# Optimization experiments

Measured on AMD Instinct MI355X. Metric: run time of the kernel, lower is better.

The kernel has to match this reference:

```python
import jax, jax.numpy as jnp
import numpy as np

TOP_K = 400
IGNORE = 255


def setup_inputs() -> dict:
    key = jax.random.key(0)
    k = jax.random.split(key, 6)
    B, C, H, W = 16, 3, 768, 768
    D, He, We = 64, 192, 192
    return {
        "outputs": jax.random.normal(k[0], (B, C, H, W), jnp.float32),
        "embeddings": jax.random.normal(k[1], (B, D, He, We), jnp.float32),
        "class_labels": jax.random.randint(k[2], (B, H, W), 0, 3, jnp.int32),
        "outputs_aug": jax.random.normal(k[3], (B, C, H, W), jnp.float32),
        "embeddings_aug": jax.random.normal(k[4], (B, D, He, We), jnp.float32),
        "class_labels_aug": jax.random.randint(k[5], (B, H, W), 0, 3, jnp.int32),
    }


def _nearest_down(x, He, We):
    # torch F.interpolate(mode='nearest') with integer downscale factor == strided slice
    sH = x.shape[-2] // He
    sW = x.shape[-1] // We
    return x[..., ::sH, ::sW]


def _forward(outputs, embeddings, outputs_aug, embeddings_aug, class_labels):
    B, C, H, W = outputs.shape
    D, He, We = embeddings.shape[1], embeddings.shape[2], embeddings.shape[3]

    # --- CrossEntropy(ignore_index=255), per-sample mean, averaged over batch ---
    logp = jax.nn.log_softmax(outputs, axis=1)                      # [B,C,H,W]
    valid = class_labels != IGNORE                                   # [B,H,W]
    lbl = jnp.where(valid, class_labels, 0).astype(jnp.int32)
    nll = -jnp.take_along_axis(logp, lbl[:, None], axis=1)[:, 0]     # [B,H,W]
    loss_ce = ((nll * valid).sum((1, 2)) / jnp.maximum(valid.sum((1, 2)), 1)).mean()

    # --- confidence / prediction maps, downsampled to embedding resolution ---
    def conf_seg(o):
        p = jax.nn.softmax(o, axis=1)
        return p.max(axis=1), p.argmax(axis=1)

    conf, seg = conf_seg(outputs)
    conf_a, seg_a = conf_seg(outputs_aug)
    segd = _nearest_down(seg, He, We)
    confd = _nearest_down(conf, He, We)
    segd_a = _nearest_down(seg_a, He, We)
    confd_a = _nearest_down(conf_a, He, We)

    def per_sample(emb, emb_a, sg, cf, sg_a, cf_a):
        ef = emb.reshape(D, -1)                                      # [D,P]
        efa = emb_a.reshape(D, -1)
        n = ef / jnp.linalg.norm(ef, axis=0, keepdims=True)          # unit columns
        na = efa / jnp.linalg.norm(efa, axis=0, keepdims=True)
        sgf, cff = sg.ravel(), cf.ravel()
        sgfa, cffa = sg_a.ravel(), cf_a.ravel()

        # ---- class 1 (ths=0.8): sort masked pixels by channel-mean, take top_k ----
        m1 = (sgf == 1) & (cff > 0.8)
        m1a = (sgfa == 1) & (cffa > 0.8)

        def topk_sel(nrm, ef_, m):
            keyv = jnp.where(m, ef_.mean(0), jnp.inf)  # unmasked -> +inf, sorted last
            idx = jnp.argsort(keyv)[:TOP_K]
            return nrm[:, idx]                         # [D,TOP_K], already unit-norm

        s1 = topk_sel(n, ef, m1)
        s1a = topk_sel(na, efa, m1a)
        d1 = 1.0 - (s1.T @ s1a).mean()                 # mean pairwise cosine distance
        v1 = (m1.sum() > TOP_K) & (m1a.sum() > TOP_K)

        # ---- class 2 (ths=0.6): all masked pixels; mean over pairs of cos-sim
        # equals dot of masked means of unit vectors (exact identity) ----
        m2 = (sgf == 2) & (cff > 0.6)
        m2a = (sgfa == 2) & (cffa > 0.6)
        mu = (n * m2).sum(1) / jnp.maximum(m2.sum(), 1)
        mua = (na * m2a).sum(1) / jnp.maximum(m2a.sum(), 1)
        d2 = 1.0 - mu @ mua
        v2 = (m2.sum() > 0) & (m2a.sum() > 0)
        return d1, v1, d2, v2

    d1, v1, d2, v2 = jax.vmap(per_sample)(embeddings, embeddings_aug, segd, confd, segd_a, confd_a)
    cnt = v1.sum() + v2.sum()
    loss_matching = (jnp.where(v1, d1, 0.0).sum() + jnp.where(v2, d2, 0.0).sum()) / jnp.maximum(cnt, 1)
    loss = loss_ce + 2.0 * loss_matching
    return loss, loss_ce, loss_matching


def reference(outputs, embeddings, class_labels, outputs_aug, embeddings_aug, class_labels_aug):
    # class_labels_aug does not enter the loss in the original code (aug CE is built but never added)
    return _forward(outputs, embeddings, outputs_aug, embeddings_aug, class_labels)
```

## Files before the change

### kernel.cpp

```cpp
#include <hip/hip_runtime.h>
#include <cstdint>
#include <cstddef>

#define Bn 16
#define Cn 3
#define Hn 768
#define Wn 768
#define Dn 64
#define HEn 192
#define WEn 192
#define Pn (HEn * WEn)
#define HWn (Hn * Wn)
#define TOPK 400
#define SENTK 0xFFFFFFFFu
#define PAD 16
#define PXB 128

struct Ws {
  float ce_sum[Bn][PAD];
  int   ce_cnt[Bn][PAD];
  int   cnt1[2][Bn][PAD];
  int   cnt2[2][Bn][PAD];
  float mu2[2][Bn][Dn][PAD];
  float mu1[2][Bn][Dn][PAD];
  int   nsel[2][Bn];
  int   idxl[2][Bn][TOPK];
  unsigned keys[2][Bn][Pn];
};
#define INIT_WORDS (256 + 256 + 512 + 512 + 32768 + 32768)
static_assert(offsetof(Ws, nsel) == (size_t)INIT_WORDS * 4, "ws layout");
static_assert(sizeof(Ws) < (size_t)6 * 1024 * 1024, "ws small");

__global__ void init_kernel(Ws* ws) {
  unsigned* w = (unsigned*)ws;
  int t = blockIdx.x * blockDim.x + threadIdx.x;
  for (int i = t; i < INIT_WORDS; i += gridDim.x * blockDim.x) w[i] = 0u;
}

__device__ __forceinline__ float wave_sum_f(float s) {
#pragma unroll
  for (int off = 32; off; off >>= 1) s += __shfl_down(s, off);
  return s;
}
__device__ __forceinline__ int wave_sum_i(int s) {
#pragma unroll
  for (int off = 32; off; off >>= 1) s += __shfl_down(s, off);
  return s;
}

__global__ void ce_kernel(const float* __restrict__ out, const int* __restrict__ lab,
                          Ws* __restrict__ ws) {
  int b = blockIdx.y;
  const int NT = 144 * 256;
  int t = blockIdx.x * 256 + threadIdx.x;
  const float* base = out + (size_t)b * Cn * HWn;
  const int* lb_base = lab + (size_t)b * HWn;
  float s = 0.f; int c = 0;
#pragma unroll
  for (int it = 0; it < 4; it++) {
    int p4 = (t + it * NT) * 4;
    float4 a0 = *(const float4*)(base + p4);
    float4 a1 = *(const float4*)(base + HWn + p4);
    float4 a2 = *(const float4*)(base + 2 * HWn + p4);
    int4 lb = *(const int4*)(lb_base + p4);
    float x0s[4] = {a0.x, a0.y, a0.z, a0.w};
    float x1s[4] = {a1.x, a1.y, a1.z, a1.w};
    float x2s[4] = {a2.x, a2.y, a2.z, a2.w};
    int ls[4] = {lb.x, lb.y, lb.z, lb.w};
#pragma unroll
    for (int k = 0; k < 4; k++) {
      int l = ls[k];
      if (l != 255) {
        float x0 = x0s[k], x1 = x1s[k], x2 = x2s[k];
        float m = fmaxf(x0, fmaxf(x1, x2));
        float lse = m + __logf(__expf(x0 - m) + __expf(x1 - m) + __expf(x2 - m));
        float xl = (l == 0) ? x0 : ((l == 1) ? x1 : x2);
        s += lse - xl;
        c += 1;
      }
    }
  }
  s = wave_sum_f(s);
  c = wave_sum_i(c);
  __shared__ float ss[4];
  __shared__ int sc[4];
  int wid = threadIdx.x >> 6;
  if ((threadIdx.x & 63) == 0) { ss[wid] = s; sc[wid] = c; }
  __syncthreads();
  if (threadIdx.x == 0) {
    atomicAdd(&ws->ce_sum[b][0], ss[0] + ss[1] + ss[2] + ss[3]);
    atomicAdd(&ws->ce_cnt[b][0], sc[0] + sc[1] + sc[2] + sc[3]);
  }
}

__global__ void main_kernel(const float* __restrict__ o0, const float* __restrict__ o1,
                            const float* __restrict__ e0, const float* __restrict__ e1,
                            Ws* __restrict__ ws) {
  int arr = blockIdx.z;
  int b = blockIdx.y;
  int lane = threadIdx.x & 63, wv = threadIdx.x >> 6;
  int p0 = blockIdx.x * PXB;
  int pa = p0 + 2 * lane;

  const float* e = (arr ? e1 : e0) + ((size_t)b * Dn + wv * 16) * Pn;
  float va[16], vb[16];
  float sum0 = 0.f, sum1 = 0.f, sq0 = 0.f, sq1 = 0.f;
#pragma unroll
  for (int k = 0; k < 16; k++) {
    float2 x = *(const float2*)(e + (size_t)k * Pn + pa);
    va[k] = x.x; vb[k] = x.y;
    sum0 += x.x; sq0 += x.x * x.x;
    sum1 += x.y; sq1 += x.y * x.y;
  }

  __shared__ float psum[4][PXB], psq[4][PXB];
  __shared__ float sscale[PXB];
  *(float2*)&psum[wv][2 * lane] = make_float2(sum0, sum1);
  *(float2*)&psq[wv][2 * lane] = make_float2(sq0, sq1);
  __syncthreads();

  if (wv == 0) {
    const float* o = (arr ? o1 : o0) + (size_t)b * Cn * HWn;
    unsigned kb[2]; float sc[2]; bool m1f[2], m2f[2];
#pragma unroll
    for (int h = 0; h < 2; h++) {
      int px = 2 * lane + h;
      int p = p0 + px;
      float ts = psum[0][px] + psum[1][px] + psum[2][px] + psum[3][px];
      float tq = psq[0][px] + psq[1][px] + psq[2][px] + psq[3][px];
      int i = p / WEn, j = p - i * WEn;
      int q = (4 * i) * Wn + 4 * j;
      float x0 = o[q], x1 = o[q + HWn], x2 = o[q + 2 * HWn];
      int sgc = 0; float m = x0;
      if (x1 > m) { m = x1; sgc = 1; }
      if (x2 > m) { m = x2; sgc = 2; }
      float conf = 1.0f / (__expf(x0 - m) + __expf(x1 - m) + __expf(x2 - m));
      bool m1 = (sgc == 1) && (conf > 0.8f);
      bool m2 = (sgc == 2) && (conf > 0.6f);
      unsigned kbv = SENTK;
      if (m1) {
        unsigned u = __float_as_uint(ts);
        kbv = (u & 0x80000000u) ? ~u : (u | 0x80000000u);
        if (kbv == SENTK) kbv--;
      }
      kb[h] = kbv;
      sc[h] = m2 ? rsqrtf(tq) : 0.f;
      m1f[h] = m1; m2f[h] = m2;
    }
    *(uint2*)&ws->keys[arr][b][pa] = make_uint2(kb[0], kb[1]);
    *(float2*)&sscale[2 * lane] = make_float2(sc[0], sc[1]);
    unsigned long long b10 = __ballot(m1f[0]), b11 = __ballot(m1f[1]);
    unsigned long long b20 = __ballot(m2f[0]), b21 = __ballot(m2f[1]);
    if (lane == 0) {
      int c1 = (int)__popcll(b10) + (int)__popcll(b11);
      int c2 = (int)__popcll(b20) + (int)__popcll(b21);
      if (c1) atomicAdd(&ws->cnt1[arr][b][0], c1);
      if (c2) atomicAdd(&ws->cnt2[arr][b][0], c2);
    }
  }
  __syncthreads();

  float2 s2 = *(const float2*)&sscale[2 * lane];
  float rv = 0.f;
#pragma unroll
  for (int k = 0; k < 16; k++) {
    float x = va[k] * s2.x + vb[k] * s2.y;
#pragma unroll
    for (int off = 1; off < 64; off <<= 1) x += __shfl_xor(x, off);
    if (lane == k) rv = x;
  }
  if (lane < 16 && rv != 0.f)
    atomicAdd(&ws->mu2[arr][b][wv * 16 + lane][0], rv);
}

__global__ void __launch_bounds__(1024) select_kernel(Ws* __restrict__ ws) {
  int arr = blockIdx.x >> 4;
  int b = blockIdx.x & 15;
  int tid = threadIdx.x;
  const uint4* __restrict__ keys4 = (const uint4*)ws->keys[arr][b];
  int c1 = ws->cnt1[arr][b][0];
  if (c1 <= TOPK) {
    if (tid == 0) ws->nsel[arr][b] = 0;
    return;
  }
  __shared__ int hist[2048];
  __shared__ int super[128];
  __shared__ int tieBuf[256];
  __shared__ unsigned sPrefix;
  __shared__ int sKRem, nBelow, nTie;
  if (tid == 0) { sPrefix = 0u; sKRem = TOPK; }

  const int shifts[3] = {21, 10, 0};
  const unsigned bmask[3] = {2047u, 2047u, 1023u};
  const int nbins[3] = {2048, 2048, 1024};

  for (int lvl = 0; lvl < 3; lvl++) {
    hist[tid] = 0;
    hist[tid + 1024] = 0;
    __syncthreads();
    unsigned pref = sPrefix;
    int shift = shifts[lvl];
    unsigned bm = bmask[lvl];
#pragma unroll
    for (int it = 0; it < 9; it++) {
      uint4 u4 = keys4[it * 1024 + tid];
      unsigned us[4] = {u4.x, u4.y, u4.z, u4.w};
#pragma unroll
      for (int k = 0; k < 4; k++) {
        unsigned u = us[k];
        if (u == SENTK) continue;
        if (lvl == 1 && (u >> 21) != (pref >> 21)) continue;
        if (lvl == 2 && (u >> 10) != (pref >> 10)) continue;
        atomicAdd(&hist[(u >> shift) & bm], 1);
      }
    }
    __syncthreads();
    int SB = nbins[lvl] >> 7;
    if (tid < 128) {
      int s = 0;
      for (int k = 0; k < SB; k++) s += hist[tid * SB + k];
      super[tid] = s;
    }
    __syncthreads();
    if (tid == 0) {
      int k = sKRem, cum = 0, sb = 127;
      for (int t = 0; t < 128; t++) {
        if (cum + super[t] >= k) { sb = t; break; }
        cum += super[t];
      }
      int j = sb * SB + SB - 1;
      for (int t = sb * SB; t < sb * SB + SB; t++) {
        if (cum + hist[t] >= k) { j = t; k -= cum; break; }
        cum += hist[t];
      }
      sKRem = k;
      sPrefix = pref | ((unsigned)j << shift);
    }
    __syncthreads();
  }
  unsigned T = sPrefix;
  int kRem = sKRem;
  if (tid == 0) { nBelow = 0; nTie = 0; }
  __syncthreads();
  int* idxl = ws->idxl[arr][b];
#pragma unroll
  for (int it = 0; it < 9; it++) {
    uint4 u4 = keys4[it * 1024 + tid];
    unsigned us[4] = {u4.x, u4.y, u4.z, u4.w};
#pragma unroll
    for (int k = 0; k < 4; k++) {
      unsigned u = us[k];
      int p = (it * 1024 + tid) * 4 + k;
      if (u < T) {
        int pos = atomicAdd(&nBelow, 1);
        if (pos < TOPK) idxl[pos] = p;
      } else if (u == T) {
        int tp = atomicAdd(&nTie, 1);
        if (tp < 256) tieBuf[tp] = p;
      }
    }
  }
  __syncthreads();
  if (tid == 0) {
    int nb = nBelow;
    int tn = nTie < 256 ? nTie : 256;
    int take = kRem < tn ? kRem : tn;
    for (int r = 0; r < take; r++) {
      int mi = r;
      for (int t = r + 1; t < tn; t++)
        if (tieBuf[t] < tieBuf[mi]) mi = t;
      int tmp = tieBuf[r]; tieBuf[r] = tieBuf[mi]; tieBuf[mi] = tmp;
      if (nb + r < TOPK) idxl[nb + r] = tieBuf[r];
    }
    int ns = nb + take;
    ws->nsel[arr][b] = ns > TOPK ? TOPK : ns;
  }
}

__global__ void accum1_kernel(const float* __restrict__ e0, const float* __restrict__ e1,
                              Ws* __restrict__ ws) {
  int arr = blockIdx.y >> 4;
  int b = blockIdx.y & 15;
  int chunk = blockIdx.x;
  int ns = ws->nsel[arr][b];
  if (chunk * 64 >= ns) return;
  int lane = threadIdx.x & 63, wv = threadIdx.x >> 6;
  int t = chunk * 64 + lane;
  bool valid = t < ns;
  int p = valid ? ws->idxl[arr][b][t] : 0;
  const float* e = (arr ? e1 : e0) + ((size_t)b * Dn + wv * 16) * Pn;
  float v[16]; float sq = 0.f;
#pragma unroll
  for (int k = 0; k < 16; k++) {
    float x = e[(size_t)k * Pn + p];
    v[k] = x; sq += x * x;
  }
  __shared__ float psq[4][64];
  psq[wv][lane] = sq;
  __syncthreads();
  float tq = psq[0][lane] + psq[1][lane] + psq[2][lane] + psq[3][lane];
  float s = valid ? rsqrtf(tq) : 0.f;
  float rv = 0.f;
#pragma unroll
  for (int k = 0; k < 16; k++) {
    float x = v[k] * s;
#pragma unroll
    for (int off = 1; off < 64; off <<= 1) x += __shfl_xor(x, off);
    if (lane == k) rv = x;
  }
  if (lane < 16 && rv != 0.f)
    atomicAdd(&ws->mu1[arr][b][wv * 16 + lane][0], rv);
}

__global__ void final_kernel(Ws* __restrict__ ws, float* __restrict__ out) {
  int t = threadIdx.x;
  float ce = 0.f, num = 0.f;
  int cnt = 0;
  if (t < Bn) {
    int cc = ws->ce_cnt[t][0];
    ce = ws->ce_sum[t][0] / (float)(cc > 1 ? cc : 1);
    int c1o = ws->cnt1[0][t][0], c1a = ws->cnt1[1][t][0];
    if (c1o > TOPK && c1a > TOPK) {
      float dot = 0.f;
      for (int d = 0; d < Dn; d++) dot += ws->mu1[0][t][d][0] * ws->mu1[1][t][d][0];
      num += 1.f - dot / ((float)TOPK * (float)TOPK);
      cnt += 1;
    }
    int c2o = ws->cnt2[0][t][0], c2a = ws->cnt2[1][t][0];
    if (c2o > 0 && c2a > 0) {
      float dot = 0.f;
      for (int d = 0; d < Dn; d++) dot += ws->mu2[0][t][d][0] * ws->mu2[1][t][d][0];
      float den = (float)(c2o > 1 ? c2o : 1) * (float)(c2a > 1 ? c2a : 1);
      num += 1.f - dot / den;
      cnt += 1;
    }
  }
#pragma unroll
  for (int off = 32; off; off >>= 1) {
    ce += __shfl_down(ce, off);
    num += __shfl_down(num, off);
    cnt += __shfl_down(cnt, off);
  }
  if (t == 0) {
    float loss_ce = ce / (float)Bn;
    float lm = num / (float)(cnt > 1 ? cnt : 1);
    out[0] = loss_ce + 2.f * lm;
    out[1] = loss_ce;
    out[2] = lm;
  }
}

extern "C" void kernel_launch(void* const* d_in, const int* in_sizes, int n_in,
                              void* d_out, int out_size, void* d_ws, size_t ws_size,
                              hipStream_t stream) {
  const float* outputs      = (const float*)d_in[0];
  const float* embeddings   = (const float*)d_in[1];
  const int*   class_labels = (const int*)d_in[2];
  const float* outputs_aug  = (const float*)d_in[3];
  const float* emb_aug      = (const float*)d_in[4];
  Ws* ws = (Ws*)d_ws;
  float* out = (float*)d_out;

  init_kernel<<<32, 256, 0, stream>>>(ws);
  ce_kernel<<<dim3(144, Bn), 256, 0, stream>>>(outputs, class_labels, ws);
  main_kernel<<<dim3(Pn / PXB, Bn, 2), 256, 0, stream>>>(outputs, outputs_aug,
                                                         embeddings, emb_aug, ws);
  select_kernel<<<32, 1024, 0, stream>>>(ws);
  accum1_kernel<<<dim3(7, 32), 256, 0, stream>>>(embeddings, emb_aug, ws);
  final_kernel<<<1, 64, 0, stream>>>(ws, out);
}
```

Baseline: 532.4 us.

## Restructure main kernel into per-wave pixel loop with register accumulation of class-2 means

The main kernel now has each wave handle 256 pixels over 8 iterations, with each half-wave reading 32 embedding channels per pixel. Channel sums and squared norms are combined with a single cross-half shuffle, which replaces the shared-memory reduction and both block-wide barriers. Class-2 contributions are accumulated in registers across iterations and reduced once per wave, cutting the per-block shuffle reductions and atomics on mu2. The cost is higher register pressure from 64 live floats per thread, a far smaller grid (36x16x2 blocks), and only 32-pixel-wide coalesced loads per row.

Result: no change. 540.4 us (+1.5%).

```diff
diff --git a/kernel.cpp b/kernel.cpp
--- a/kernel.cpp
+++ b/kernel.cpp
@@ -14,7 +14,6 @@
 #define TOPK 400
 #define SENTK 0xFFFFFFFFu
 #define PAD 16
-#define PXB 128
 
 struct Ws {
   float ce_sum[Bn][PAD];
@@ -93,41 +92,31 @@
   }
 }
 
-__global__ void main_kernel(const float* __restrict__ o0, const float* __restrict__ o1,
-                            const float* __restrict__ e0, const float* __restrict__ e1,
-                            Ws* __restrict__ ws) {
-  int arr = blockIdx.z;
-  int b = blockIdx.y;
-  int lane = threadIdx.x & 63, wv = threadIdx.x >> 6;
-  int p0 = blockIdx.x * PXB;
-  int pa = p0 + 2 * lane;
-
-  const float* e = (arr ? e1 : e0) + ((size_t)b * Dn + wv * 16) * Pn;
-  float va[16], vb[16];
-  float sum0 = 0.f, sum1 = 0.f, sq0 = 0.f, sq1 = 0.f;
-#pragma unroll
-  for (int k = 0; k < 16; k++) {
-    float2 x = *(const float2*)(e + (size_t)k * Pn + pa);
-    va[k] = x.x; vb[k] = x.y;
-    sum0 += x.x; sq0 += x.x * x.x;
-    sum1 += x.y; sq1 += x.y * x.y;
-  }
-
-  __shared__ float psum[4][PXB], psq[4][PXB];
-  __shared__ float sscale[PXB];
-  *(float2*)&psum[wv][2 * lane] = make_float2(sum0, sum1);
-  *(float2*)&psq[wv][2 * lane] = make_float2(sq0, sq1);
-  __syncthreads();
-
-  if (wv == 0) {
-    const float* o = (arr ? o1 : o0) + (size_t)b * Cn * HWn;
-    unsigned kb[2]; float sc[2]; bool m1f[2], m2f[2];
-#pragma unroll
-    for (int h = 0; h < 2; h++) {
-      int px = 2 * lane + h;
-      int p = p0 + px;
-      float ts = psum[0][px] + psum[1][px] + psum[2][px] + psum[3][px];
-      float tq = psq[0][px] + psq[1][px] + psq[2][px] + psq[3][px];
+__global__ void __launch_bounds__(256, 4)
+main_kernel(const float* __restrict__ o0, const float* __restrict__ o1,
+            const float* __restrict__ e0, const float* __restrict__ e1,
+            Ws* __restrict__ ws) {
+  const int arr = blockIdx.z;
+  const int b = blockIdx.y;
+  const int lane = threadIdx.x & 63, wv = threadIdx.x >> 6;
+  const int wave_id = blockIdx.x * 4 + wv;
+  const int l31 = lane & 31;
+  const int half = lane >> 5;
+  const float* e = (arr ? e1 : e0) + (size_t)(b * Dn + half * 32) * (size_t)Pn;
+  const float* o = (arr ? o1 : o0) + (size_t)b * Cn * HWn;
+  unsigned* __restrict__ keys = ws->keys[arr][b];
+
+  float acc[32];
+#pragma unroll
+  for (int k = 0; k < 32; k++) acc[k] = 0.f;
+  int c1a = 0, c2a = 0;
+
+#pragma unroll 1
+  for (int g = 0; g < 8; g++) {
+    const int p = wave_id * 256 + g * 32 + l31;
+
+    bool m1 = false, m2 = false;
+    if (half == 0) {
       int i = p / WEn, j = p - i * WEn;
       int q = (4 * i) * Wn + 4 * j;
       float x0 = o[q], x1 = o[q + HWn], x2 = o[q + 2 * HWn];
@@ -135,42 +124,55 @@
       if (x1 > m) { m = x1; sgc = 1; }
       if (x2 > m) { m = x2; sgc = 2; }
       float conf = 1.0f / (__expf(x0 - m) + __expf(x1 - m) + __expf(x2 - m));
-      bool m1 = (sgc == 1) && (conf > 0.8f);
-      bool m2 = (sgc == 2) && (conf > 0.6f);
+      m1 = (sgc == 1) && (conf > 0.8f);
+      m2 = (sgc == 2) && (conf > 0.6f);
+    }
+
+    const float* ep = e + p;
+    float v[32];
+    float s = 0.f, sq = 0.f;
+#pragma unroll
+    for (int k = 0; k < 32; k++) {
+      float x = ep[(size_t)k * Pn];
+      v[k] = x; s += x; sq += x * x;
+    }
+    s += __shfl_xor(s, 32);
+    sq += __shfl_xor(sq, 32);
+
+    float sc = 0.f;
+    if (half == 0) {
       unsigned kbv = SENTK;
       if (m1) {
-        unsigned u = __float_as_uint(ts);
+        unsigned u = __float_as_uint(s);
         kbv = (u & 0x80000000u) ? ~u : (u | 0x80000000u);
         if (kbv == SENTK) kbv--;
       }
-      kb[h] = kbv;
-      sc[h] = m2 ? rsqrtf(tq) : 0.f;
-      m1f[h] = m1; m2f[h] = m2;
-    }
-    *(uint2*)&ws->keys[arr][b][pa] = make_uint2(kb[0], kb[1]);
-    *(float2*)&sscale[2 * lane] = make_float2(sc[0], sc[1]);
-    unsigned long long b10 = __ballot(m1f[0]), b11 = __ballot(m1f[1]);
-    unsigned long long b20 = __ballot(m2f[0]), b21 = __ballot(m2f[1]);
-    if (lane == 0) {
-      int c1 = (int)__popcll(b10) + (int)__popcll(b11);
-      int c2 = (int)__popcll(b20) + (int)__popcll(b21);
-      if (c1) atomicAdd(&ws->cnt1[arr][b][0], c1);
-      if (c2) atomicAdd(&ws->cnt2[arr][b][0], c2);
-    }
-  }
-  __syncthreads();
-
-  float2 s2 = *(const float2*)&sscale[2 * lane];
-  float rv = 0.f;
-#pragma unroll
-  for (int k = 0; k < 16; k++) {
-    float x = va[k] * s2.x + vb[k] * s2.y;
-#pragma unroll
-    for (int off = 1; off < 64; off <<= 1) x += __shfl_xor(x, off);
-    if (lane == k) rv = x;
-  }
-  if (lane < 16 && rv != 0.f)
-    atomicAdd(&ws->mu2[arr][b][wv * 16 + lane][0], rv);
+      keys[p] = kbv;
+      if (m2) sc = rsqrtf(sq);
+    }
+    float scu = __shfl_xor(sc, 32);
+    if (half) sc = scu;
+
+#pragma unroll
+    for (int k = 0; k < 32; k++) acc[k] = fmaf(v[k], sc, acc[k]);
+
+    unsigned long long b1 = __ballot(m1), b2 = __ballot(m2);
+    c1a += (int)__popcll(b1);
+    c2a += (int)__popcll(b2);
+  }
+
+#pragma unroll
+  for (int k = 0; k < 32; k++) {
+    float x = acc[k];
+#pragma unroll
+    for (int off = 1; off < 32; off <<= 1) x += __shfl_xor(x, off);
+    if (l31 == k && x != 0.f)
+      atomicAdd(&ws->mu2[arr][b][half * 32 + k][0], x);
+  }
+  if (lane == 0) {
+    if (c1a) atomicAdd(&ws->cnt1[arr][b][0], c1a);
+    if (c2a) atomicAdd(&ws->cnt2[arr][b][0], c2a);
+  }
 }
 
 __global__ void __launch_bounds__(1024) select_kernel(Ws* __restrict__ ws) {
@@ -363,8 +365,8 @@
 
   init_kernel<<<32, 256, 0, stream>>>(ws);
   ce_kernel<<<dim3(144, Bn), 256, 0, stream>>>(outputs, class_labels, ws);
-  main_kernel<<<dim3(Pn / PXB, Bn, 2), 256, 0, stream>>>(outputs, outputs_aug,
-                                                         embeddings, emb_aug, ws);
+  main_kernel<<<dim3(36, Bn, 2), 256, 0, stream>>>(outputs, outputs_aug,
+                                                   embeddings, emb_aug, ws);
   select_kernel<<<32, 1024, 0, stream>>>(ws);
   accum1_kernel<<<dim3(7, 32), 256, 0, stream>>>(embeddings, emb_aug, ws);
   final_kernel<<<1, 64, 0, stream>>>(ws, out);
```

## Process four pixel chunks per block in main_kernel with register accumulation

Applied to the files above, without the earlier changes.

Each main_kernel block now loops over four 128-pixel chunks and accumulates the class-2 masked embedding sums in registers. The 16 shuffle reductions and the mu2 and count atomics are therefore issued once per block instead of once per chunk. The next chunk's logits are prefetched while the current chunk is processed, and launch bounds are set to 256 threads with 6 blocks per unit. The grid becomes four times smaller, which lowers parallelism and adds a serial loop with extra barriers per block.

Result: no change. 526.0 us (-1.2%).

```diff
diff --git a/kernel.cpp b/kernel.cpp
--- a/kernel.cpp
+++ b/kernel.cpp
@@ -15,6 +15,7 @@
 #define SENTK 0xFFFFFFFFu
 #define PAD 16
 #define PXB 128
+#define CHUNKS 4
 
 struct Ws {
   float ce_sum[Bn][PAD];
@@ -93,84 +94,117 @@
   }
 }
 
-__global__ void main_kernel(const float* __restrict__ o0, const float* __restrict__ o1,
-                            const float* __restrict__ e0, const float* __restrict__ e1,
-                            Ws* __restrict__ ws) {
+__global__ void __launch_bounds__(256, 6)
+main_kernel(const float* __restrict__ o0, const float* __restrict__ o1,
+            const float* __restrict__ e0, const float* __restrict__ e1,
+            Ws* __restrict__ ws) {
   int arr = blockIdx.z;
   int b = blockIdx.y;
   int lane = threadIdx.x & 63, wv = threadIdx.x >> 6;
-  int p0 = blockIdx.x * PXB;
-  int pa = p0 + 2 * lane;
-
+  int base_p = blockIdx.x * (PXB * CHUNKS);
+
+  const float* o = (arr ? o1 : o0) + (size_t)b * Cn * HWn;
   const float* e = (arr ? e1 : e0) + ((size_t)b * Dn + wv * 16) * Pn;
-  float va[16], vb[16];
-  float sum0 = 0.f, sum1 = 0.f, sq0 = 0.f, sq1 = 0.f;
-#pragma unroll
-  for (int k = 0; k < 16; k++) {
-    float2 x = *(const float2*)(e + (size_t)k * Pn + pa);
-    va[k] = x.x; vb[k] = x.y;
-    sum0 += x.x; sq0 += x.x * x.x;
-    sum1 += x.y; sq1 += x.y * x.y;
-  }
 
   __shared__ float psum[4][PXB], psq[4][PXB];
   __shared__ float sscale[PXB];
-  *(float2*)&psum[wv][2 * lane] = make_float2(sum0, sum1);
-  *(float2*)&psq[wv][2 * lane] = make_float2(sq0, sq1);
-  __syncthreads();
-
+
+  float acc[16];
+#pragma unroll
+  for (int k = 0; k < 16; k++) acc[k] = 0.f;
+  int c1a = 0, c2a = 0;
+
+  float px0[2], px1[2], px2[2];
   if (wv == 0) {
-    const float* o = (arr ? o1 : o0) + (size_t)b * Cn * HWn;
-    unsigned kb[2]; float sc[2]; bool m1f[2], m2f[2];
 #pragma unroll
     for (int h = 0; h < 2; h++) {
-      int px = 2 * lane + h;
-      int p = p0 + px;
-      float ts = psum[0][px] + psum[1][px] + psum[2][px] + psum[3][px];
-      float tq = psq[0][px] + psq[1][px] + psq[2][px] + psq[3][px];
+      int p = base_p + 2 * lane + h;
       int i = p / WEn, j = p - i * WEn;
       int q = (4 * i) * Wn + 4 * j;
-      float x0 = o[q], x1 = o[q + HWn], x2 = o[q + 2 * HWn];
-      int sgc = 0; float m = x0;
-      if (x1 > m) { m = x1; sgc = 1; }
-      if (x2 > m) { m = x2; sgc = 2; }
-      float conf = 1.0f / (__expf(x0 - m) + __expf(x1 - m) + __expf(x2 - m));
-      bool m1 = (sgc == 1) && (conf > 0.8f);
-      bool m2 = (sgc == 2) && (conf > 0.6f);
-      unsigned kbv = SENTK;
-      if (m1) {
-        unsigned u = __float_as_uint(ts);
-        kbv = (u & 0x80000000u) ? ~u : (u | 0x80000000u);
-        if (kbv == SENTK) kbv--;
-      }
-      kb[h] = kbv;
-      sc[h] = m2 ? rsqrtf(tq) : 0.f;
-      m1f[h] = m1; m2f[h] = m2;
-    }
-    *(uint2*)&ws->keys[arr][b][pa] = make_uint2(kb[0], kb[1]);
-    *(float2*)&sscale[2 * lane] = make_float2(sc[0], sc[1]);
-    unsigned long long b10 = __ballot(m1f[0]), b11 = __ballot(m1f[1]);
-    unsigned long long b20 = __ballot(m2f[0]), b21 = __ballot(m2f[1]);
-    if (lane == 0) {
-      int c1 = (int)__popcll(b10) + (int)__popcll(b11);
-      int c2 = (int)__popcll(b20) + (int)__popcll(b21);
-      if (c1) atomicAdd(&ws->cnt1[arr][b][0], c1);
-      if (c2) atomicAdd(&ws->cnt2[arr][b][0], c2);
-    }
-  }
-  __syncthreads();
-
-  float2 s2 = *(const float2*)&sscale[2 * lane];
+      px0[h] = o[q]; px1[h] = o[q + HWn]; px2[h] = o[q + 2 * HWn];
+    }
+  }
+
+#pragma unroll 1
+  for (int c = 0; c < CHUNKS; c++) {
+    int p0 = base_p + c * PXB;
+    int pa = p0 + 2 * lane;
+
+    float va[16], vb[16];
+    float sum0 = 0.f, sum1 = 0.f, sq0 = 0.f, sq1 = 0.f;
+#pragma unroll
+    for (int k = 0; k < 16; k++) {
+      float2 x = *(const float2*)(e + (size_t)k * Pn + pa);
+      va[k] = x.x; vb[k] = x.y;
+      sum0 += x.x; sq0 += x.x * x.x;
+      sum1 += x.y; sq1 += x.y * x.y;
+    }
+    *(float2*)&psum[wv][2 * lane] = make_float2(sum0, sum1);
+    *(float2*)&psq[wv][2 * lane] = make_float2(sq0, sq1);
+    __syncthreads();
+
+    if (wv == 0) {
+      unsigned kb[2]; float sc[2]; bool m1f[2], m2f[2];
+#pragma unroll
+      for (int h = 0; h < 2; h++) {
+        int px = 2 * lane + h;
+        float ts = psum[0][px] + psum[1][px] + psum[2][px] + psum[3][px];
+        float tq = psq[0][px] + psq[1][px] + psq[2][px] + psq[3][px];
+        float x0 = px0[h], x1 = px1[h], x2 = px2[h];
+        int sgc = 0; float m = x0;
+        if (x1 > m) { m = x1; sgc = 1; }
+        if (x2 > m) { m = x2; sgc = 2; }
+        float conf = 1.0f / (__expf(x0 - m) + __expf(x1 - m) + __expf(x2 - m));
+        bool m1 = (sgc == 1) && (conf > 0.8f);
+        bool m2 = (sgc == 2) && (conf > 0.6f);
+        unsigned kbv = SENTK;
+        if (m1) {
+          unsigned u = __float_as_uint(ts);
+          kbv = (u & 0x80000000u) ? ~u : (u | 0x80000000u);
+          if (kbv == SENTK) kbv--;
+        }
+        kb[h] = kbv;
+        sc[h] = m2 ? rsqrtf(tq) : 0.f;
+        m1f[h] = m1; m2f[h] = m2;
+      }
+      *(uint2*)&ws->keys[arr][b][pa] = make_uint2(kb[0], kb[1]);
+      *(float2*)&sscale[2 * lane] = make_float2(sc[0], sc[1]);
+      unsigned long long b10 = __ballot(m1f[0]), b11 = __ballot(m1f[1]);
+      unsigned long long b20 = __ballot(m2f[0]), b21 = __ballot(m2f[1]);
+      c1a += (int)__popcll(b10) + (int)__popcll(b11);
+      c2a += (int)__popcll(b20) + (int)__popcll(b21);
+      if (c + 1 < CHUNKS) {
+#pragma unroll
+        for (int h = 0; h < 2; h++) {
+          int p = p0 + PXB + 2 * lane + h;
+          int i = p / WEn, j = p - i * WEn;
+          int q = (4 * i) * Wn + 4 * j;
+          px0[h] = o[q]; px1[h] = o[q + HWn]; px2[h] = o[q + 2 * HWn];
+        }
+      }
+    }
+    __syncthreads();
+
+    float2 s2 = *(const float2*)&sscale[2 * lane];
+#pragma unroll
+    for (int k = 0; k < 16; k++)
+      acc[k] += va[k] * s2.x + vb[k] * s2.y;
+  }
+
   float rv = 0.f;
 #pragma unroll
   for (int k = 0; k < 16; k++) {
-    float x = va[k] * s2.x + vb[k] * s2.y;
+    float x = acc[k];
 #pragma unroll
     for (int off = 1; off < 64; off <<= 1) x += __shfl_xor(x, off);
     if (lane == k) rv = x;
   }
   if (lane < 16 && rv != 0.f)
     atomicAdd(&ws->mu2[arr][b][wv * 16 + lane][0], rv);
+  if (wv == 0 && lane == 0) {
+    if (c1a) atomicAdd(&ws->cnt1[arr][b][0], c1a);
+    if (c2a) atomicAdd(&ws->cnt2[arr][b][0], c2a);
+  }
 }
 
 __global__ void __launch_bounds__(1024) select_kernel(Ws* __restrict__ ws) {
@@ -363,8 +397,8 @@
 
   init_kernel<<<32, 256, 0, stream>>>(ws);
   ce_kernel<<<dim3(144, Bn), 256, 0, stream>>>(outputs, class_labels, ws);
-  main_kernel<<<dim3(Pn / PXB, Bn, 2), 256, 0, stream>>>(outputs, outputs_aug,
-                                                         embeddings, emb_aug, ws);
+  main_kernel<<<dim3(Pn / (PXB * CHUNKS), Bn, 2), 256, 0, stream>>>(
+      outputs, outputs_aug, embeddings, emb_aug, ws);
   select_kernel<<<32, 1024, 0, stream>>>(ws);
   accum1_kernel<<<dim3(7, 32), 256, 0, stream>>>(embeddings, emb_aug, ws);
   final_kernel<<<1, 64, 0, stream>>>(ws, out);
```
